# Kernel tuning notes

Hardware: AMD Instinct MI355X
Metric: run time of the kernel (lower is better)

Reference implementation:

```python
import jax, jax.numpy as jnp
import numpy as np

EPS_NORM = 1e-6  # MVLayerNorm epsilon


def _build_cayley():
    # Cl(3,0): blades as bitmasks, ordered by (grade, bitmask):
    # [1, e1, e2, e3, e12, e13, e23, e123]
    n = 3
    order = sorted(range(1 << n), key=lambda b: (bin(b).count('1'), b))
    idx = {b: i for i, b in enumerate(order)}
    C = np.zeros((8, 8, 8), dtype=np.float32)
    for a in range(8):
        for b in range(8):
            # sign from reordering basis vectors (Euclidean metric: e_i^2 = +1)
            swaps, ash = 0, a >> 1
            while ash:
                swaps += bin(ash & b).count('1')
                ash >>= 1
            C[idx[a], idx[a ^ b], idx[b]] = -1.0 if swaps % 2 else 1.0
    return C

_CAYLEY_NP = _build_cayley()
CAYLEY = jnp.asarray(_CAYLEY_NP)
# metric of each blade: scalar part of blade*blade -> [1,1,1,1,-1,-1,-1,-1]
METRIC = jnp.asarray(np.array([_CAYLEY_NP[i, 0, i] for i in range(8)], dtype=np.float32))
# blade -> grade subspace index, subspace dims [1,3,3,1]
BLADE2SUB = np.array([0, 1, 1, 1, 2, 2, 2, 3])


def mv_linear(x, w, b):
    # x: (B, in, 8); w: (out, in, 4); b: (out,) added to scalar blade only
    wb = w[:, :, BLADE2SUB]                      # (out, in, 8) per-blade weight
    y = jnp.einsum('bmi,nmi->bni', x, wb)        # (B, out, 8)
    return y.at[..., 0].add(b)


def mv_layernorm(x, a):
    # quadratic form per channel: q = sum_i g_i * x_i^2, shape (B, C, 1)
    q = jnp.einsum('bci,i,bci->bc', x, METRIC, x)[..., None]
    norm = (q * q + 1e-16) ** 0.25               # smooth sqrt(|q|)
    norm = norm.mean(axis=1, keepdims=True) + EPS_NORM  # (B, 1, 1)
    return a[None, :, None] * x / norm


def setup_inputs() -> dict:
    key = jax.random.key(0)
    ks = jax.random.split(key, 8)
    N, C_IN, C_HID, NSUB = 4096, 512, 512, 4
    s = 1.0 / np.sqrt(C_IN)
    return {
        'x': jax.random.normal(ks[0], (N, C_IN, 8), jnp.float32),
        'w1': jax.random.normal(ks[1], (C_HID, C_IN, NSUB), jnp.float32) * s,
        'b1': jax.random.normal(ks[2], (C_HID,), jnp.float32) * 0.02,
        'w2': jax.random.normal(ks[3], (C_HID, C_IN, NSUB), jnp.float32) * s,
        'b2': jax.random.normal(ks[4], (C_HID,), jnp.float32) * 0.02,
        'w3': jax.random.normal(ks[5], (C_IN, C_HID, NSUB), jnp.float32) * s,
        'b3': jax.random.normal(ks[6], (C_IN,), jnp.float32) * 0.02,
        'a_norm': jax.random.normal(ks[7], (C_IN,), jnp.float32) * 0.1 + 1.0,
    }


def reference(x, w1, b1, w2, b2, w3, b3, a_norm):
    x_l = mv_linear(x, w1, b1)                       # (N, hid, 8)
    x_r = mv_linear(x, w2, b2)                       # (N, hid, 8)
    gp = jnp.einsum('bni,ijk,bnk->bnj', x_l, CAYLEY, x_r)  # sparse Cayley product
    y = mv_linear(gp, w3, b3)                        # (N, in, 8)
    return mv_layernorm(y, a_norm)
```

## Files before the change

kernel.cpp:

```cpp
#include <hip/hip_runtime.h>
#include <hip/hip_bf16.h>
#include <cstdint>
#include <cstddef>

typedef __bf16 bf16;
typedef __bf16 bf16x2_t __attribute__((ext_vector_type(2)));
typedef __bf16 bf16x4_t __attribute__((ext_vector_type(4)));
typedef __bf16 bf16x8_t __attribute__((ext_vector_type(8)));
typedef float  f32x2_t  __attribute__((ext_vector_type(2)));
typedef float  f32x4_t  __attribute__((ext_vector_type(4)));

#define NTOK 4096
#define CH   512
#define SLICE (NTOK*CH)
#define WSLICE (CH*CH)

#define AS1 __attribute__((address_space(1)))
#define AS3 __attribute__((address_space(3)))

__device__ __forceinline__ void gl_lds16(const void* g, void* l) {
    __builtin_amdgcn_global_load_lds((const AS1 unsigned int*)g,
                                     (AS3 unsigned int*)l, 16, 0, 0);
}

__global__ __launch_bounds__(256) void k_convert_x(const float* __restrict__ x,
                                                   bf16* __restrict__ xb) {
    int p = blockIdx.x * 256 + threadIdx.x;
    const f32x4_t* x4 = (const f32x4_t*)x;
    f32x4_t v0 = x4[2*p];
    f32x4_t v1 = x4[2*p+1];
    xb[0*SLICE + p] = (bf16)v0.x;
    xb[1*SLICE + p] = (bf16)v0.y;
    xb[2*SLICE + p] = (bf16)v0.z;
    xb[3*SLICE + p] = (bf16)v0.w;
    xb[4*SLICE + p] = (bf16)v1.x;
    xb[5*SLICE + p] = (bf16)v1.y;
    xb[6*SLICE + p] = (bf16)v1.z;
    xb[7*SLICE + p] = (bf16)v1.w;
}

__global__ __launch_bounds__(256) void k_convert_w(const float* __restrict__ w1,
                                                   const float* __restrict__ w2,
                                                   const float* __restrict__ w3,
                                                   bf16* __restrict__ w1b,
                                                   bf16* __restrict__ w2b,
                                                   bf16* __restrict__ w3b) {
    int p = blockIdx.x * 256 + threadIdx.x;
    const float* w = (blockIdx.y == 0) ? w1 : (blockIdx.y == 1) ? w2 : w3;
    bf16* wb       = (blockIdx.y == 0) ? w1b : (blockIdx.y == 1) ? w2b : w3b;
    f32x4_t v = ((const f32x4_t*)w)[p];
    wb[0*WSLICE + p] = (bf16)v.x;
    wb[1*WSLICE + p] = (bf16)v.y;
    wb[2*WSLICE + p] = (bf16)v.z;
    wb[3*WSLICE + p] = (bf16)v.w;
}

__global__ __launch_bounds__(256, 2) void k_gemm12(const bf16* __restrict__ xb,
                                                   const bf16* __restrict__ w1b,
                                                   const bf16* __restrict__ w2b,
                                                   bf16* __restrict__ xl,
                                                   bf16* __restrict__ xr) {
    const int blade = blockIdx.z;
    const int sub = (blade == 0) ? 0 : (blade < 4) ? 1 : (blade < 7) ? 2 : 3;
    const bf16* A  = xb  + (size_t)blade * SLICE;
    const bf16* B1 = w1b + (size_t)sub * WSLICE;
    const bf16* B2 = w2b + (size_t)sub * WSLICE;
    const int tm = blockIdx.x * 128, tn = blockIdx.y * 128;

    __shared__ __align__(1024) bf16 lsA[128 * 64];
    char* lsAc = (char*)lsA;

    const int t = threadIdx.x, lane = t & 63, wid = t >> 6;
    const int waveM = (wid >> 1) * 64, waveN = (wid & 1) * 64;

    const int srow = wid * 32 + (lane >> 3);
    const int sswz = ((lane & 7) ^ (lane >> 3)) * 8;
    const bf16* Ag = A + (size_t)(tm + srow) * CH + sswz;
    const int ldsq = wid * 4096;

    const int xorv  = (lane & 7) << 4;
    const int kbase = (lane >> 4) * 16;

    const bf16* B1t = B1 + (size_t)(tn + waveN + (lane & 15)) * CH + (lane >> 4) * 8;
    const bf16* B2t = B2 + (size_t)(tn + waveN + (lane & 15)) * CH + (lane >> 4) * 8;

    f32x4_t accL[4][4] = {};
    f32x4_t accR[4][4] = {};

    #pragma unroll 1
    for (int kt = 0; kt < 8; ++kt) {
        const int k0 = kt * 64;
        __syncthreads();
        #pragma unroll
        for (int q = 0; q < 4; ++q)
            gl_lds16(Ag + (size_t)q * 8 * CH + k0, lsAc + ldsq + q * 1024);
        __syncthreads();
        #pragma unroll
        for (int kk = 0; kk < 2; ++kk) {
            const int koff = kk * 64 + kbase;
            const int gk   = k0 + kk * 32;
            bf16x8_t af[4], b1f[4], b2f[4];
            #pragma unroll
            for (int mf = 0; mf < 4; ++mf) {
                int row = waveM + mf * 16 + (lane & 15);
                af[mf] = *(const bf16x8_t*)(lsAc + row * 128 + (koff ^ xorv));
            }
            #pragma unroll
            for (int nf = 0; nf < 4; ++nf) {
                b1f[nf] = *(const bf16x8_t*)(B1t + (size_t)nf * 16 * CH + gk);
                b2f[nf] = *(const bf16x8_t*)(B2t + (size_t)nf * 16 * CH + gk);
            }
            #pragma unroll
            for (int mf = 0; mf < 4; ++mf)
                #pragma unroll
                for (int nf = 0; nf < 4; ++nf) {
                    accL[mf][nf] = __builtin_amdgcn_mfma_f32_16x16x32_bf16(
                        b1f[nf], af[mf], accL[mf][nf], 0, 0, 0);
                    accR[mf][nf] = __builtin_amdgcn_mfma_f32_16x16x32_bf16(
                        b2f[nf], af[mf], accR[mf][nf], 0, 0, 0);
                }
        }
    }

    bf16* O1 = xl + (size_t)blade * SLICE;
    bf16* O2 = xr + (size_t)blade * SLICE;
    #pragma unroll
    for (int mf = 0; mf < 4; ++mf) {
        size_t rowoff = (size_t)(tm + waveM + mf * 16 + (lane & 15)) * CH;
        #pragma unroll
        for (int nf = 0; nf < 4; ++nf) {
            int ch = tn + waveN + nf * 16 + (lane >> 4) * 4;
            bf16x4_t v1, v2;
            #pragma unroll
            for (int r = 0; r < 4; ++r) {
                v1[r] = (bf16)accL[mf][nf][r];
                v2[r] = (bf16)accR[mf][nf][r];
            }
            *(bf16x4_t*)(O1 + rowoff + ch) = v1;
            *(bf16x4_t*)(O2 + rowoff + ch) = v2;
        }
    }
}

__global__ __launch_bounds__(256, 2) void k_gemm3(const bf16* __restrict__ gp,
                                                  const bf16* __restrict__ w3b,
                                                  bf16* __restrict__ yb) {
    const int blade = blockIdx.z;
    const int sub = (blade == 0) ? 0 : (blade < 4) ? 1 : (blade < 7) ? 2 : 3;
    const bf16* A = gp  + (size_t)blade * SLICE;
    const bf16* B = w3b + (size_t)sub * WSLICE;
    const int tm = blockIdx.x * 128, tn = blockIdx.y * 128;

    __shared__ __align__(1024) bf16 lsA[128 * 64];
    char* lsAc = (char*)lsA;

    const int t = threadIdx.x, lane = t & 63, wid = t >> 6;
    const int waveM = (wid >> 1) * 64, waveN = (wid & 1) * 64;

    const int srow = wid * 32 + (lane >> 3);
    const int sswz = ((lane & 7) ^ (lane >> 3)) * 8;
    const bf16* Ag = A + (size_t)(tm + srow) * CH + sswz;
    const int ldsq = wid * 4096;

    const int xorv  = (lane & 7) << 4;
    const int kbase = (lane >> 4) * 16;

    const bf16* Bt = B + (size_t)(tn + waveN + (lane & 15)) * CH + (lane >> 4) * 8;

    f32x4_t acc[4][4] = {};

    #pragma unroll 1
    for (int kt = 0; kt < 8; ++kt) {
        const int k0 = kt * 64;
        __syncthreads();
        #pragma unroll
        for (int q = 0; q < 4; ++q)
            gl_lds16(Ag + (size_t)q * 8 * CH + k0, lsAc + ldsq + q * 1024);
        __syncthreads();
        #pragma unroll
        for (int kk = 0; kk < 2; ++kk) {
            const int koff = kk * 64 + kbase;
            const int gk   = k0 + kk * 32;
            bf16x8_t af[4], bf[4];
            #pragma unroll
            for (int mf = 0; mf < 4; ++mf) {
                int row = waveM + mf * 16 + (lane & 15);
                af[mf] = *(const bf16x8_t*)(lsAc + row * 128 + (koff ^ xorv));
            }
            #pragma unroll
            for (int nf = 0; nf < 4; ++nf)
                bf[nf] = *(const bf16x8_t*)(Bt + (size_t)nf * 16 * CH + gk);
            #pragma unroll
            for (int mf = 0; mf < 4; ++mf)
                #pragma unroll
                for (int nf = 0; nf < 4; ++nf)
                    acc[mf][nf] = __builtin_amdgcn_mfma_f32_16x16x32_bf16(
                        bf[nf], af[mf], acc[mf][nf], 0, 0, 0);
        }
    }

    bf16* O = yb + (size_t)blade * SLICE;
    #pragma unroll
    for (int mf = 0; mf < 4; ++mf) {
        size_t rowoff = (size_t)(tm + waveM + mf * 16 + (lane & 15)) * CH;
        #pragma unroll
        for (int nf = 0; nf < 4; ++nf) {
            int ch = tn + waveN + nf * 16 + (lane >> 4) * 4;
            bf16x4_t v;
            #pragma unroll
            for (int r = 0; r < 4; ++r) v[r] = (bf16)acc[mf][nf][r];
            *(bf16x4_t*)(O + rowoff + ch) = v;
        }
    }
}

__global__ __launch_bounds__(256) void k_gp(const bf16* __restrict__ xl,
                                            const bf16* __restrict__ xr,
                                            const float* __restrict__ b1,
                                            const float* __restrict__ b2,
                                            bf16* __restrict__ gp) {
    int p = (blockIdx.x * 256 + threadIdx.x) * 4;
    float l[8][4], r[8][4], g[8][4];
    #pragma unroll
    for (int i = 0; i < 8; ++i) {
        bf16x4_t lv = *(const bf16x4_t*)(xl + (size_t)i * SLICE + p);
        bf16x4_t rv = *(const bf16x4_t*)(xr + (size_t)i * SLICE + p);
        #pragma unroll
        for (int v = 0; v < 4; ++v) { l[i][v] = (float)lv[v]; r[i][v] = (float)rv[v]; g[i][v] = 0.f; }
    }
    int n0 = p & (CH - 1);
    f32x4_t b1v = *(const f32x4_t*)(b1 + n0);
    f32x4_t b2v = *(const f32x4_t*)(b2 + n0);
    #pragma unroll
    for (int v = 0; v < 4; ++v) { l[0][v] += b1v[v]; r[0][v] += b2v[v]; }

    const int IDX[8] = {0, 1, 2, 4, 3, 5, 6, 7};
    #pragma unroll
    for (int a = 0; a < 8; ++a) {
        #pragma unroll
        for (int b = 0; b < 8; ++b) {
            int e = ((((a >> 1) ^ (a >> 2)) & b) & 1) ^ (((a >> 2) & (b >> 1)) & 1);
            int j = IDX[a ^ b], ia = IDX[a], ib = IDX[b];
            #pragma unroll
            for (int v = 0; v < 4; ++v)
                g[j][v] += e ? (-l[ia][v] * r[ib][v]) : (l[ia][v] * r[ib][v]);
        }
    }
    #pragma unroll
    for (int i = 0; i < 8; ++i) {
        bf16x4_t gv;
        #pragma unroll
        for (int v = 0; v < 4; ++v) gv[v] = (bf16)g[i][v];
        *(bf16x4_t*)(gp + (size_t)i * SLICE + p) = gv;
    }
}

__global__ __launch_bounds__(256) void k_ln(const bf16* __restrict__ y,
                                            const float* __restrict__ b3,
                                            const float* __restrict__ an,
                                            float* __restrict__ out) {
    int b = blockIdx.x, t = threadIdx.x;
    int c0 = t * 2;
    size_t base = (size_t)b * CH + c0;
    float yv[2][8];
    #pragma unroll
    for (int i = 0; i < 8; ++i) {
        bf16x2_t v = *(const bf16x2_t*)(y + (size_t)i * SLICE + base);
        yv[0][i] = (float)v[0];
        yv[1][i] = (float)v[1];
    }
    f32x2_t b3v = *(const f32x2_t*)(b3 + c0);
    float nsum = 0.f;
    #pragma unroll
    for (int h = 0; h < 2; ++h) {
        yv[h][0] += b3v[h];
        float q = yv[h][0]*yv[h][0] + yv[h][1]*yv[h][1] + yv[h][2]*yv[h][2] + yv[h][3]*yv[h][3]
                - yv[h][4]*yv[h][4] - yv[h][5]*yv[h][5] - yv[h][6]*yv[h][6] - yv[h][7]*yv[h][7];
        nsum += sqrtf(sqrtf(q * q + 1e-16f));
    }
    #pragma unroll
    for (int off = 32; off; off >>= 1) nsum += __shfl_xor(nsum, off);
    __shared__ float red[4];
    if ((t & 63) == 0) red[t >> 6] = nsum;
    __syncthreads();
    float denom = (red[0] + red[1] + red[2] + red[3]) * (1.f / 512.f) + 1e-6f;
    float inv = 1.f / denom;
    f32x2_t anv = *(const f32x2_t*)(an + c0);
    float out16[16];
    #pragma unroll
    for (int h = 0; h < 2; ++h) {
        float s = anv[h] * inv;
        #pragma unroll
        for (int i = 0; i < 8; ++i) out16[h * 8 + i] = yv[h][i] * s;
    }
    size_t base8 = base * 8;
    #pragma unroll
    for (int j = 0; j < 4; ++j)
        *(f32x4_t*)(out + base8 + j * 4) = *(f32x4_t*)(out16 + j * 4);
}

extern "C" void kernel_launch(void* const* d_in, const int* in_sizes, int n_in,
                              void* d_out, int out_size, void* d_ws, size_t ws_size,
                              hipStream_t stream) {
    (void)in_sizes; (void)n_in; (void)out_size; (void)ws_size;
    const float* x  = (const float*)d_in[0];
    const float* w1 = (const float*)d_in[1];
    const float* b1 = (const float*)d_in[2];
    const float* w2 = (const float*)d_in[3];
    const float* b2 = (const float*)d_in[4];
    const float* w3 = (const float*)d_in[5];
    const float* b3 = (const float*)d_in[6];
    const float* an = (const float*)d_in[7];

    char* ws = (char*)d_ws;
    bf16*  xb  = (bf16*)(ws);
    bf16*  xl  = (bf16*)(ws + 33554432);
    bf16*  xr  = (bf16*)(ws + 67108864);
    bf16*  yb  = (bf16*)(ws + 33554432);
    bf16*  w1b = (bf16*)(ws + 100663296);
    bf16*  w2b = (bf16*)(ws + 102760448);
    bf16*  w3b = (bf16*)(ws + 104857600);

    k_convert_x<<<SLICE / 256, 256, 0, stream>>>(x, xb);
    dim3 gw(WSLICE / 256, 3);
    k_convert_w<<<gw, 256, 0, stream>>>(w1, w2, w3, w1b, w2b, w3b);

    dim3 gg(NTOK / 128, CH / 128, 8);
    k_gemm12<<<gg, 256, 0, stream>>>(xb, w1b, w2b, xl, xr);
    k_gp<<<SLICE / 4 / 256, 256, 0, stream>>>(xl, xr, b1, b2, xb );
    k_gemm3<<<gg, 256, 0, stream>>>(xb, w3b, yb);
    k_ln<<<NTOK, 256, 0, stream>>>(yb, b3, an, (float*)d_out);
}
```

Before: 305.4 us.

## Stage weight tiles through LDS and enlarge gemm3 M-tile to 256

The first two GEMMs now copy the W1 and W2 weight tiles into swizzled shared memory with async global-to-LDS loads, where before each wave read them straight from global memory. The third GEMM also stages its weight tile in LDS and doubles its M tile to 256 rows, so each wave holds 8x4 accumulators and the grid is halved. This cuts redundant uncoalesced global B loads and raises reuse per block. The cost is more LDS per block and more accumulator registers in gemm3, which may reduce occupancy.

```diff
diff --git a/kernel.cpp b/kernel.cpp
--- a/kernel.cpp
+++ b/kernel.cpp
@@ -67,22 +67,25 @@
     const bf16* B2 = w2b + (size_t)sub * WSLICE;
     const int tm = blockIdx.x * 128, tn = blockIdx.y * 128;
 
-    __shared__ __align__(1024) bf16 lsA[128 * 64];
-    char* lsAc = (char*)lsA;
+    __shared__ __align__(1024) bf16 lsA [128 * 64];
+    __shared__ __align__(1024) bf16 lsB1[128 * 64];
+    __shared__ __align__(1024) bf16 lsB2[128 * 64];
+    char* lsAc  = (char*)lsA;
+    char* lsB1c = (char*)lsB1;
+    char* lsB2c = (char*)lsB2;
 
     const int t = threadIdx.x, lane = t & 63, wid = t >> 6;
     const int waveM = (wid >> 1) * 64, waveN = (wid & 1) * 64;
 
     const int srow = wid * 32 + (lane >> 3);
-    const int sswz = ((lane & 7) ^ (lane >> 3)) * 8;
-    const bf16* Ag = A + (size_t)(tm + srow) * CH + sswz;
+    const int sswz = ((lane & 7) ^ (lane >> 3 & 7)) * 8;
+    const bf16* Ag  = A  + (size_t)(tm + srow) * CH + sswz;
+    const bf16* B1g = B1 + (size_t)(tn + srow) * CH + sswz;
+    const bf16* B2g = B2 + (size_t)(tn + srow) * CH + sswz;
     const int ldsq = wid * 4096;
 
     const int xorv  = (lane & 7) << 4;
     const int kbase = (lane >> 4) * 16;
-
-    const bf16* B1t = B1 + (size_t)(tn + waveN + (lane & 15)) * CH + (lane >> 4) * 8;
-    const bf16* B2t = B2 + (size_t)(tn + waveN + (lane & 15)) * CH + (lane >> 4) * 8;
 
     f32x4_t accL[4][4] = {};
     f32x4_t accR[4][4] = {};
@@ -92,13 +95,15 @@
         const int k0 = kt * 64;
         __syncthreads();
         #pragma unroll
-        for (int q = 0; q < 4; ++q)
-            gl_lds16(Ag + (size_t)q * 8 * CH + k0, lsAc + ldsq + q * 1024);
+        for (int q = 0; q < 4; ++q) {
+            gl_lds16(Ag  + (size_t)q * 8 * CH + k0, lsAc  + ldsq + q * 1024);
+            gl_lds16(B1g + (size_t)q * 8 * CH + k0, lsB1c + ldsq + q * 1024);
+            gl_lds16(B2g + (size_t)q * 8 * CH + k0, lsB2c + ldsq + q * 1024);
+        }
         __syncthreads();
         #pragma unroll
         for (int kk = 0; kk < 2; ++kk) {
             const int koff = kk * 64 + kbase;
-            const int gk   = k0 + kk * 32;
             bf16x8_t af[4], b1f[4], b2f[4];
             #pragma unroll
             for (int mf = 0; mf < 4; ++mf) {
@@ -107,8 +112,9 @@
             }
             #pragma unroll
             for (int nf = 0; nf < 4; ++nf) {
-                b1f[nf] = *(const bf16x8_t*)(B1t + (size_t)nf * 16 * CH + gk);
-                b2f[nf] = *(const bf16x8_t*)(B2t + (size_t)nf * 16 * CH + gk);
+                int row = waveN + nf * 16 + (lane & 15);
+                b1f[nf] = *(const bf16x8_t*)(lsB1c + row * 128 + (koff ^ xorv));
+                b2f[nf] = *(const bf16x8_t*)(lsB2c + row * 128 + (koff ^ xorv));
             }
             #pragma unroll
             for (int mf = 0; mf < 4; ++mf)
@@ -149,49 +155,52 @@
     const int sub = (blade == 0) ? 0 : (blade < 4) ? 1 : (blade < 7) ? 2 : 3;
     const bf16* A = gp  + (size_t)blade * SLICE;
     const bf16* B = w3b + (size_t)sub * WSLICE;
-    const int tm = blockIdx.x * 128, tn = blockIdx.y * 128;
-
-    __shared__ __align__(1024) bf16 lsA[128 * 64];
+    const int tm = blockIdx.x * 256, tn = blockIdx.y * 128;
+
+    __shared__ __align__(1024) bf16 lsA[256 * 64];
+    __shared__ __align__(1024) bf16 lsB[128 * 64];
     char* lsAc = (char*)lsA;
+    char* lsBc = (char*)lsB;
 
     const int t = threadIdx.x, lane = t & 63, wid = t >> 6;
-    const int waveM = (wid >> 1) * 64, waveN = (wid & 1) * 64;
-
-    const int srow = wid * 32 + (lane >> 3);
-    const int sswz = ((lane & 7) ^ (lane >> 3)) * 8;
-    const bf16* Ag = A + (size_t)(tm + srow) * CH + sswz;
-    const int ldsq = wid * 4096;
+    const int waveM = (wid >> 1) * 128, waveN = (wid & 1) * 64;
+
+    const int sswz = ((t & 7) ^ (t >> 3 & 7)) * 8;
+    const bf16* Ag = A + (size_t)(tm + (t >> 3)) * CH + sswz;
+    const bf16* Bg = B + (size_t)(tn + (t >> 3)) * CH + sswz;
 
     const int xorv  = (lane & 7) << 4;
     const int kbase = (lane >> 4) * 16;
 
-    const bf16* Bt = B + (size_t)(tn + waveN + (lane & 15)) * CH + (lane >> 4) * 8;
-
-    f32x4_t acc[4][4] = {};
+    f32x4_t acc[8][4] = {};
 
     #pragma unroll 1
     for (int kt = 0; kt < 8; ++kt) {
         const int k0 = kt * 64;
         __syncthreads();
         #pragma unroll
+        for (int q = 0; q < 8; ++q)
+            gl_lds16(Ag + (size_t)q * 32 * CH + k0, lsAc + q * 4096 + t * 16);
+        #pragma unroll
         for (int q = 0; q < 4; ++q)
-            gl_lds16(Ag + (size_t)q * 8 * CH + k0, lsAc + ldsq + q * 1024);
+            gl_lds16(Bg + (size_t)q * 32 * CH + k0, lsBc + q * 4096 + t * 16);
         __syncthreads();
         #pragma unroll
         for (int kk = 0; kk < 2; ++kk) {
             const int koff = kk * 64 + kbase;
-            const int gk   = k0 + kk * 32;
-            bf16x8_t af[4], bf[4];
-            #pragma unroll
-            for (int mf = 0; mf < 4; ++mf) {
+            bf16x8_t af[8], bf[4];
+            #pragma unroll
+            for (int mf = 0; mf < 8; ++mf) {
                 int row = waveM + mf * 16 + (lane & 15);
                 af[mf] = *(const bf16x8_t*)(lsAc + row * 128 + (koff ^ xorv));
             }
             #pragma unroll
-            for (int nf = 0; nf < 4; ++nf)
-                bf[nf] = *(const bf16x8_t*)(Bt + (size_t)nf * 16 * CH + gk);
-            #pragma unroll
-            for (int mf = 0; mf < 4; ++mf)
+            for (int nf = 0; nf < 4; ++nf) {
+                int row = waveN + nf * 16 + (lane & 15);
+                bf[nf] = *(const bf16x8_t*)(lsBc + row * 128 + (koff ^ xorv));
+            }
+            #pragma unroll
+            for (int mf = 0; mf < 8; ++mf)
                 #pragma unroll
                 for (int nf = 0; nf < 4; ++nf)
                     acc[mf][nf] = __builtin_amdgcn_mfma_f32_16x16x32_bf16(
@@ -201,7 +210,7 @@
 
     bf16* O = yb + (size_t)blade * SLICE;
     #pragma unroll
-    for (int mf = 0; mf < 4; ++mf) {
+    for (int mf = 0; mf < 8; ++mf) {
         size_t rowoff = (size_t)(tm + waveM + mf * 16 + (lane & 15)) * CH;
         #pragma unroll
         for (int nf = 0; nf < 4; ++nf) {
@@ -325,9 +334,10 @@
     dim3 gw(WSLICE / 256, 3);
     k_convert_w<<<gw, 256, 0, stream>>>(w1, w2, w3, w1b, w2b, w3b);
 
-    dim3 gg(NTOK / 128, CH / 128, 8);
-    k_gemm12<<<gg, 256, 0, stream>>>(xb, w1b, w2b, xl, xr);
+    dim3 g12(NTOK / 128, CH / 128, 8);
+    k_gemm12<<<g12, 256, 0, stream>>>(xb, w1b, w2b, xl, xr);
     k_gp<<<SLICE / 4 / 256, 256, 0, stream>>>(xl, xr, b1, b2, xb );
-    k_gemm3<<<gg, 256, 0, stream>>>(xb, w3b, yb);
+    dim3 g3(NTOK / 256, CH / 128, 8);
+    k_gemm3<<<g3, 256, 0, stream>>>(xb, w3b, yb);
     k_ln<<<NTOK, 256, 0, stream>>>(yb, b3, an, (float*)d_out);
 }
```

Result: faster. 250.7 us (-17.9%).
